# Optimization experiments

Hardware: AMD Instinct MI355X
Metric: run time of the kernel (lower is better)

The kernel has to match this reference:

```python
import jax, jax.numpy as jnp
import numpy as np


def setup_inputs() -> dict:
    key = jax.random.key(0)
    k0, k1, k2, k3 = jax.random.split(key, 4)
    B, N, C, Dout = 4, 8192, 64, 128
    coords = jax.random.normal(k0, (B, N, 3), dtype=jnp.float32)
    features = jax.random.normal(k1, (B, N, C), dtype=jnp.float32)
    W1 = jax.random.normal(k2, (C + 3, Dout), dtype=jnp.float32) / jnp.sqrt(jnp.float32(C + 3))
    b1 = jnp.zeros((Dout,), dtype=jnp.float32)
    W2 = jax.random.normal(k3, (Dout, Dout), dtype=jnp.float32) / jnp.sqrt(jnp.float32(Dout))
    b2 = jnp.zeros((Dout,), dtype=jnp.float32)
    return {"coords": coords, "features": features, "W1": W1, "b1": b1,
            "W2": W2, "b2": b2, "sample_count": 2048, "k": 32}


def reference(coords, features, W1, b1, W2, b2, sample_count, k):
    B, N, _ = coords.shape
    S = min(sample_count, N)
    kk = min(k, N)
    # deterministic linspace centroid sampling (same indices for every batch)
    idx = jnp.round(jnp.linspace(0.0, N - 1, S)).astype(jnp.int32)  # [S]
    sampled = coords[:, idx]  # [B,S,3]
    # squared distances via GEMM (same topk ordering as torch.cdist)
    s2 = jnp.sum(sampled * sampled, axis=-1)          # [B,S]
    c2 = jnp.sum(coords * coords, axis=-1)            # [B,N]
    d2 = s2[:, :, None] + c2[:, None, :] - 2.0 * jnp.einsum('bsd,bnd->bsn', sampled, coords)
    _, knn_idx = jax.lax.top_k(-d2, kk)               # [B,S,kk] smallest distances
    # per-batch irregular gathers
    grouped_c = jax.vmap(lambda c, i: c[i])(coords, knn_idx)      # [B,S,kk,3]
    rel = grouped_c - sampled[:, :, None, :]                      # relative coords
    grouped_f = jax.vmap(lambda f, i: f[i])(features, knn_idx)    # [B,S,kk,C]
    g = jnp.concatenate([rel, grouped_f], axis=-1)                # [B,S,kk,C+3]
    # shared MLP: Linear -> GELU(exact) -> Linear -> GELU(exact)
    h = jax.nn.gelu(g @ W1 + b1, approximate=False)
    h = jax.nn.gelu(h @ W2 + b2, approximate=False)
    pooled = jnp.max(h, axis=2)                                   # [B,S,Dout]
    return sampled, pooled
```

## Files before the change

### kernel.cpp

```cpp
#include <hip/hip_runtime.h>
#include <math.h>

typedef unsigned int u32;
typedef unsigned long long u64;

#define BB 4
#define NN 8192
#define CC 64
#define DOUT 128
#define SS 2048
#define KSEL 32
#define CAPL 2048
#define CAP2 384
#define BREAK_CAP 128

__device__ __forceinline__ int sample_index(int s) {
    if (s == 1706) return 6826;
    const double step = 8191.0 / 2047.0;
    return (int)rint((double)s * step);
}

__device__ __forceinline__ u32 f2s(float f) {
    u32 u = __float_as_uint(f);
    return ((int)u < 0) ? ~u : (u ^ 0x80000000u);
}

__device__ __forceinline__ float gelu(float x) {
    return 0.5f * x * (1.0f + erff(x * 0.70710678118654752f));
}

__global__ __launch_bounds__(256)
__attribute__((amdgpu_waves_per_eu(4, 4)))
void k_select(const float* __restrict__ coords,
              float* __restrict__ out_sampled,
              int* __restrict__ selbuf,
              int selstride) {
    __shared__ __align__(16) u64 cand[CAPL];
    __shared__ __align__(16) u64 cand2[CAP2];
    __shared__ u32 wsum[32];
    __shared__ int sel[KSEL];
    __shared__ int s_nsel, s_ncand, s_n2;

    const int tid = threadIdx.x;
    const int lane = tid & 63;
    const int q = blockIdx.x;
    const int b = q >> 11;
    const int s = q & (SS - 1);
    const int si = sample_index(s);

    const float* cb = coords + (size_t)b * NN * 3;
    const float qx = cb[si * 3 + 0], qy = cb[si * 3 + 1], qz = cb[si * 3 + 2];
    const float q2 = __fadd_rn(__fadd_rn(__fmul_rn(qx, qx), __fmul_rn(qy, qy)), __fmul_rn(qz, qz));

    if (tid == 0) {
        float* dst = out_sampled + (size_t)q * 3;
        dst[0] = qx; dst[1] = qy; dst[2] = qz;
    }

    u32 kr[32];
#pragma unroll
    for (int i = 0; i < 32; i++) {
        int j = tid + (i << 8);
        float x = cb[j * 3 + 0], y = cb[j * 3 + 1], z = cb[j * 3 + 2];
        float n2 = __fadd_rn(__fadd_rn(__fmul_rn(x, x), __fmul_rn(y, y)), __fmul_rn(z, z));
        float dot = __fadd_rn(__fadd_rn(__fmul_rn(qx, x), __fmul_rn(qy, y)), __fmul_rn(qz, z));
        float d2 = __fsub_rn(__fadd_rn(q2, n2), __fmul_rn(2.0f, dot));
        kr[i] = f2s(d2);
    }

#define BFLY_WSUM()                                                          \
    _Pragma("unroll")                                                        \
    for (int w = 0; w < 8; w++) {                                            \
        _Pragma("unroll")                                                    \
        for (int d = 1; d < 64; d <<= 1) cnt[w] += __shfl_xor(cnt[w], d, 64);\
    }                                                                        \
    if ((tid & 63) == 0) {                                                   \
        int wv = tid >> 6;                                                   \
        _Pragma("unroll")                                                    \
        for (int w = 0; w < 8; w++) wsum[wv * 8 + w] = cnt[w];               \
    }                                                                        \
    __syncthreads();

#define SCAN_DIGIT()                                                         \
    u32 tot[8];                                                              \
    _Pragma("unroll")                                                        \
    for (int w = 0; w < 8; w++)                                              \
        tot[w] = wsum[w] + wsum[8 + w] + wsum[16 + w] + wsum[24 + w];        \
    run = 0; D = 15; cc = 0;                                                 \
    _Pragma("unroll")                                                        \
    for (int nib = 0; nib < 16; nib++) {                                     \
        int cv = (nib & 1) ? (int)(tot[nib >> 1] >> 16)                      \
                           : (int)(tot[nib >> 1] & 0xFFFFu);                 \
        if (base + run + cv >= KSEL) { D = nib; cc = cv; break; }            \
        run += cv;                                                           \
    }

    u32 pref = 0;
    int base = 0, shift = 28, c = 0;
    int p = 7;
    {
        u32 cnt[8] = {0, 0, 0, 0, 0, 0, 0, 0};
#pragma unroll
        for (int i = 0; i < 32; i++) {
            u32 nib = kr[i] >> 28;
            cnt[nib >> 1] += 1u << (16 * (nib & 1));
        }
        BFLY_WSUM()
        int run, D, cc;
        SCAN_DIGIT()
        base = run; pref = (u32)D << 28; c = cc;
        __syncthreads();
    }

    while (c > CAPL && p > 0) {
        p--;
        const int sh = 4 * p;
        const u32 hmask = 0xFFFFFFFFu << (sh + 4);
        u32 cnt[8] = {0, 0, 0, 0, 0, 0, 0, 0};
#pragma unroll
        for (int i = 0; i < 32; i++) {
            u32 kv = kr[i];
            if ((kv & hmask) == pref) {
                u32 nib = (kv >> sh) & 15u;
                cnt[nib >> 1] += 1u << (16 * (nib & 1));
            }
        }
        BFLY_WSUM()
        int run, D, cc;
        SCAN_DIGIT()
        base += run; pref |= (u32)D << sh; shift = sh; c = cc;
        __syncthreads();
    }

    if (tid == 0) { s_nsel = 0; s_ncand = 0; }
    __syncthreads();

    const u64 lmlt = (1ull << lane) - 1ull;
    {
        const u32 prefv = pref >> shift;
#pragma unroll
        for (int i = 0; i < 32; i++) {
            int j = tid + (i << 8);
            u32 kv = kr[i];
            u32 kp = kv >> shift;
            bool isS = kp < prefv;
            bool isC = kp == prefv;
            u64 bs = __ballot(isS);
            u64 bc = __ballot(isC);
            int basS = 0, basC = 0;
            if (lane == 0) {
                if (bs) basS = atomicAdd(&s_nsel, (int)__popcll(bs));
                if (bc) basC = atomicAdd(&s_ncand, (int)__popcll(bc));
            }
            basS = __shfl(basS, 0, 64);
            basC = __shfl(basC, 0, 64);
            if (isS) sel[basS + (int)__popcll(bs & lmlt)] = j;
            if (isC) {
                int pos = basC + (int)__popcll(bc & lmlt);
                if (pos < CAPL) cand[pos] = ((u64)kv << 32) | (u32)j;
            }
        }
    }
    __syncthreads();
    int nc = s_ncand; if (nc > CAPL) nc = CAPL;

    int p2 = shift >> 2;
    while (c > BREAK_CAP && p2 > 0) {
        p2--;
        const int sh = 4 * p2;
        const u32 ph = pref >> (sh + 4);
        u32 cnt[8] = {0, 0, 0, 0, 0, 0, 0, 0};
        for (int e = tid; e < nc; e += 256) {
            u32 kv = (u32)(cand[e] >> 32);
            if ((kv >> (sh + 4)) == ph) {
                u32 nib = (kv >> sh) & 15u;
                cnt[nib >> 1] += 1u << (16 * (nib & 1));
            }
        }
        BFLY_WSUM()
        int run, D, cc;
        SCAN_DIGIT()
        base += run; pref |= (u32)D << sh; shift = sh; c = cc;
        __syncthreads();
    }
#undef BFLY_WSUM
#undef SCAN_DIGIT

    if (tid == 0) s_n2 = 0;
    __syncthreads();
    {
        const u32 pv = pref >> shift;
        for (int e = tid; e < nc; e += 256) {
            u64 ent = cand[e];
            u32 kp = (u32)(ent >> 32) >> shift;
            bool isS = kp < pv;
            bool isC = kp == pv;
            u64 bs = __ballot(isS);
            u64 bc = __ballot(isC);
            int basS = 0, basC = 0;
            if (lane == 0) {
                if (bs) basS = atomicAdd(&s_nsel, (int)__popcll(bs));
                if (bc) basC = atomicAdd(&s_n2, (int)__popcll(bc));
            }
            basS = __shfl(basS, 0, 64);
            basC = __shfl(basC, 0, 64);
            if (isS) sel[basS + (int)__popcll(bs & lmlt)] = (int)(ent & 0xFFFFFFFFu);
            if (isC) {
                int pos = basC + (int)__popcll(bc & lmlt);
                if (pos < CAP2) cand2[pos] = ent;
            }
        }
    }
    __syncthreads();

    {
        const int nles = s_nsel;
        const int need = KSEL - nles;
        int n2 = s_n2; if (n2 > CAP2) n2 = CAP2;
        for (int ci = tid; ci < n2; ci += 256) {
            u64 me = cand2[ci];
            int r = 0;
            for (int m = 0; m < n2; m++) r += (cand2[m] < me) ? 1 : 0;
            if (r < need) sel[nles + r] = (int)(me & 0xFFFFFFFFu);
        }
    }
    __syncthreads();

    if (tid < KSEL) selbuf[(size_t)q * selstride + tid] = sel[tid];
}

__global__ __launch_bounds__(512) void k_mlp(const float* __restrict__ coords,
                                             const float* __restrict__ features,
                                             const float* __restrict__ w1,
                                             const float* __restrict__ b1,
                                             const float* __restrict__ w2,
                                             const float* __restrict__ b2,
                                             const int* __restrict__ selbuf,
                                             int selstride,
                                             float* __restrict__ pooled) {
    __shared__ __align__(16) unsigned char smem[32768];
    float* g    = (float*)smem;
    float* h    = (float*)smem;
    float* part = (float*)smem;
    __shared__ int sel2[2][KSEL];

    const int tid = threadIdx.x;
    const int q0 = blockIdx.x << 1;
    const int b = q0 >> 11;
    const float* cb = coords + (size_t)b * NN * 3;

    if (tid < 2 * KSEL) {
        int hq = tid >> 5;
        sel2[hq][tid & 31] = selbuf[(size_t)(q0 + hq) * selstride + (tid & 31)];
    }
    __syncthreads();

    {
        const int hq = tid >> 8;
        const int t = tid & 255;
        const int s = (q0 + hq) & (SS - 1);
        const int si = sample_index(s);
        const float qx = cb[si * 3 + 0], qy = cb[si * 3 + 1], qz = cb[si * 3 + 2];
        const int nbr = (t >> 3) & 31;
        const int cl = t & 7;
        const int n = sel2[hq][nbr];
        const float* fb = features + ((size_t)b * NN + n) * CC;
        float* gq = g + hq * 2144;
#pragma unroll
        for (int m = 0; m < 9; m++) {
            int ch = cl + (m << 3);
            if (ch < 67) {
                float v;
                if (ch < 3) v = cb[n * 3 + ch] - ((ch == 0) ? qx : (ch == 1) ? qy : qz);
                else        v = fb[ch - 3];
                gq[ch * 32 + nbr] = v;
            }
        }
    }
    __syncthreads();

    const int lane = tid & 63;
    const int chb = __builtin_amdgcn_readfirstlane((tid >> 6) << 4);
    const int hq = lane >> 5;
    const int nb = lane & 31;

    float acc[16];

    {
        const float* brow = b1 + chb;
#pragma unroll
        for (int k = 0; k < 16; k++) acc[k] = brow[k];
        const float* aA = g + hq * 2144 + nb;
        const float* w1p = w1 + chb;
        for (int c = 0; c < 67; c++) {
            float a = aA[c * 32];
            const float* wr = w1p + c * DOUT;
#pragma unroll
            for (int k = 0; k < 16; k++) acc[k] = fmaf(a, wr[k], acc[k]);
        }
    }
    __syncthreads();
    {
        float* hp = h + hq * 4096 + nb;
#pragma unroll
        for (int k = 0; k < 16; k++) hp[(chb + k) * 32] = gelu(acc[k]);
    }
    __syncthreads();

    {
        const float* brow = b2 + chb;
#pragma unroll
        for (int k = 0; k < 16; k++) acc[k] = brow[k];
        const float* aA = h + hq * 4096 + nb;
        const float* w2p = w2 + chb;
        for (int c = 0; c < DOUT; c++) {
            float a = aA[c * 32];
            const float* wr = w2p + c * DOUT;
#pragma unroll
            for (int k = 0; k < 16; k++) acc[k] = fmaf(a, wr[k], acc[k]);
        }
    }
#pragma unroll
    for (int k = 0; k < 16; k++) acc[k] = gelu(acc[k]);
    __syncthreads();
    {
        float* pp = part + hq * 4096;
#pragma unroll
        for (int k = 0; k < 16; k++) {
            int j = chb + k;
            pp[j * 32 + (nb ^ (j & 31))] = acc[k];
        }
    }
    __syncthreads();

    if (tid < 256) {
        const int hq2 = tid >> 7;
        const int ch = tid & 127;
        const float* pr = part + hq2 * 4096 + ch * 32;
        const int sw = ch & 31;
        float m = pr[0 ^ sw];
#pragma unroll
        for (int w = 1; w < 32; w++) m = fmaxf(m, pr[w ^ sw]);
        pooled[(size_t)(q0 + hq2) * DOUT + ch] = m;
    }
}

extern "C" void kernel_launch(void* const* d_in, const int* in_sizes, int n_in,
                              void* d_out, int out_size, void* d_ws, size_t ws_size,
                              hipStream_t stream) {
    const float* coords = nullptr;
    const float* features = nullptr;
    const float* W1 = nullptr;
    const float* b1 = nullptr;
    const float* W2 = nullptr;
    const float* b2 = nullptr;
    for (int i = 0; i < n_in; i++) {
        int sz = in_sizes[i];
        const float* p = (const float*)d_in[i];
        if      (sz == BB * NN * 3)     coords = p;
        else if (sz == BB * NN * CC)    features = p;
        else if (sz == (CC + 3) * DOUT) W1 = p;
        else if (sz == DOUT * DOUT)     W2 = p;
        else if (sz == DOUT)            { if (!b1) b1 = p; else b2 = p; }
    }

    float* out_sampled = (float*)d_out;
    float* out_pooled  = (float*)d_out + (size_t)BB * SS * 3;

    const size_t sel_bytes = (size_t)BB * SS * KSEL * sizeof(int);
    int* selbuf;
    int selstride;
    if (ws_size >= sel_bytes && d_ws != nullptr) {
        selbuf = (int*)d_ws;
        selstride = KSEL;
    } else {
        selbuf = (int*)out_pooled;
        selstride = DOUT;
    }

    k_select<<<dim3(BB * SS), dim3(256), 0, stream>>>(coords, out_sampled, selbuf, selstride);
    k_mlp<<<dim3((BB * SS) / 2), dim3(512), 0, stream>>>(coords, features, W1, b1, W2, b2,
                                                         selbuf, selstride, out_pooled);
}
```

Measured before the change: 422.2 us.

## Widen kNN select blocks to 512 threads and use packed FMA in MLP

The top-k selection kernel now runs 512 threads per query instead of 256, so each thread holds 16 distance keys instead of 32, with the per-wave histogram sums widened to 8 waves and the occupancy hints changed. The MLP kernel's accumulators become float2 vectors updated with elementwise FMA, so the compiler can emit packed FP32 FMA instructions. The aim is more parallelism and lower register pressure in selection, and doubled FMA throughput in the MLP. The cost is more barrier and reduction work per block in selection, and a risk that the packed form does not lower to packed instructions.

```diff
diff --git a/kernel.cpp b/kernel.cpp
--- a/kernel.cpp
+++ b/kernel.cpp
@@ -3,6 +3,7 @@
 
 typedef unsigned int u32;
 typedef unsigned long long u64;
+typedef float f32x2 __attribute__((ext_vector_type(2)));
 
 #define BB 4
 #define NN 8192
@@ -29,15 +30,15 @@
     return 0.5f * x * (1.0f + erff(x * 0.70710678118654752f));
 }
 
-__global__ __launch_bounds__(256)
-__attribute__((amdgpu_waves_per_eu(4, 4)))
+__global__ __launch_bounds__(512)
+__attribute__((amdgpu_waves_per_eu(6, 8)))
 void k_select(const float* __restrict__ coords,
               float* __restrict__ out_sampled,
               int* __restrict__ selbuf,
               int selstride) {
     __shared__ __align__(16) u64 cand[CAPL];
     __shared__ __align__(16) u64 cand2[CAP2];
-    __shared__ u32 wsum[32];
+    __shared__ u32 wsum[64];
     __shared__ int sel[KSEL];
     __shared__ int s_nsel, s_ncand, s_n2;
 
@@ -57,10 +58,10 @@
         dst[0] = qx; dst[1] = qy; dst[2] = qz;
     }
 
-    u32 kr[32];
-#pragma unroll
-    for (int i = 0; i < 32; i++) {
-        int j = tid + (i << 8);
+    u32 kr[16];
+#pragma unroll
+    for (int i = 0; i < 16; i++) {
+        int j = tid + (i << 9);
         float x = cb[j * 3 + 0], y = cb[j * 3 + 1], z = cb[j * 3 + 2];
         float n2 = __fadd_rn(__fadd_rn(__fmul_rn(x, x), __fmul_rn(y, y)), __fmul_rn(z, z));
         float dot = __fadd_rn(__fadd_rn(__fmul_rn(qx, x), __fmul_rn(qy, y)), __fmul_rn(qz, z));
@@ -84,8 +85,12 @@
 #define SCAN_DIGIT()                                                         \
     u32 tot[8];                                                              \
     _Pragma("unroll")                                                        \
-    for (int w = 0; w < 8; w++)                                              \
-        tot[w] = wsum[w] + wsum[8 + w] + wsum[16 + w] + wsum[24 + w];        \
+    for (int w = 0; w < 8; w++) {                                            \
+        u32 t = 0;                                                           \
+        _Pragma("unroll")                                                    \
+        for (int v = 0; v < 8; v++) t += wsum[v * 8 + w];                    \
+        tot[w] = t;                                                          \
+    }                                                                        \
     run = 0; D = 15; cc = 0;                                                 \
     _Pragma("unroll")                                                        \
     for (int nib = 0; nib < 16; nib++) {                                     \
@@ -101,7 +106,7 @@
     {
         u32 cnt[8] = {0, 0, 0, 0, 0, 0, 0, 0};
 #pragma unroll
-        for (int i = 0; i < 32; i++) {
+        for (int i = 0; i < 16; i++) {
             u32 nib = kr[i] >> 28;
             cnt[nib >> 1] += 1u << (16 * (nib & 1));
         }
@@ -118,7 +123,7 @@
         const u32 hmask = 0xFFFFFFFFu << (sh + 4);
         u32 cnt[8] = {0, 0, 0, 0, 0, 0, 0, 0};
 #pragma unroll
-        for (int i = 0; i < 32; i++) {
+        for (int i = 0; i < 16; i++) {
             u32 kv = kr[i];
             if ((kv & hmask) == pref) {
                 u32 nib = (kv >> sh) & 15u;
@@ -139,8 +144,8 @@
     {
         const u32 prefv = pref >> shift;
 #pragma unroll
-        for (int i = 0; i < 32; i++) {
-            int j = tid + (i << 8);
+        for (int i = 0; i < 16; i++) {
+            int j = tid + (i << 9);
             u32 kv = kr[i];
             u32 kp = kv >> shift;
             bool isS = kp < prefv;
@@ -170,7 +175,7 @@
         const int sh = 4 * p2;
         const u32 ph = pref >> (sh + 4);
         u32 cnt[8] = {0, 0, 0, 0, 0, 0, 0, 0};
-        for (int e = tid; e < nc; e += 256) {
+        for (int e = tid; e < nc; e += 512) {
             u32 kv = (u32)(cand[e] >> 32);
             if ((kv >> (sh + 4)) == ph) {
                 u32 nib = (kv >> sh) & 15u;
@@ -190,7 +195,7 @@
     __syncthreads();
     {
         const u32 pv = pref >> shift;
-        for (int e = tid; e < nc; e += 256) {
+        for (int e = tid; e < nc; e += 512) {
             u64 ent = cand[e];
             u32 kp = (u32)(ent >> 32) >> shift;
             bool isS = kp < pv;
@@ -217,7 +222,7 @@
         const int nles = s_nsel;
         const int need = KSEL - nles;
         int n2 = s_n2; if (n2 > CAP2) n2 = CAP2;
-        for (int ci = tid; ci < n2; ci += 256) {
+        for (int ci = tid; ci < n2; ci += 512) {
             u64 me = cand2[ci];
             int r = 0;
             for (int m = 0; m < n2; m++) r += (cand2[m] < me) ? 1 : 0;
@@ -284,51 +289,58 @@
     const int hq = lane >> 5;
     const int nb = lane & 31;
 
-    float acc[16];
-
-    {
-        const float* brow = b1 + chb;
-#pragma unroll
-        for (int k = 0; k < 16; k++) acc[k] = brow[k];
+    f32x2 acc2[8];
+
+    {
+        const f32x2* br2 = (const f32x2*)(b1 + chb);
+#pragma unroll
+        for (int k = 0; k < 8; k++) acc2[k] = br2[k];
         const float* aA = g + hq * 2144 + nb;
         const float* w1p = w1 + chb;
         for (int c = 0; c < 67; c++) {
             float a = aA[c * 32];
-            const float* wr = w1p + c * DOUT;
-#pragma unroll
-            for (int k = 0; k < 16; k++) acc[k] = fmaf(a, wr[k], acc[k]);
+            f32x2 av = {a, a};
+            const f32x2* wr2 = (const f32x2*)(w1p + c * DOUT);
+#pragma unroll
+            for (int k = 0; k < 8; k++)
+                acc2[k] = __builtin_elementwise_fma(av, wr2[k], acc2[k]);
         }
     }
     __syncthreads();
     {
         float* hp = h + hq * 4096 + nb;
 #pragma unroll
-        for (int k = 0; k < 16; k++) hp[(chb + k) * 32] = gelu(acc[k]);
-    }
-    __syncthreads();
-
-    {
-        const float* brow = b2 + chb;
-#pragma unroll
-        for (int k = 0; k < 16; k++) acc[k] = brow[k];
+        for (int k = 0; k < 8; k++) {
+            hp[(chb + 2 * k) * 32]     = gelu(acc2[k].x);
+            hp[(chb + 2 * k + 1) * 32] = gelu(acc2[k].y);
+        }
+    }
+    __syncthreads();
+
+    {
+        const f32x2* br2 = (const f32x2*)(b2 + chb);
+#pragma unroll
+        for (int k = 0; k < 8; k++) acc2[k] = br2[k];
         const float* aA = h + hq * 4096 + nb;
         const float* w2p = w2 + chb;
         for (int c = 0; c < DOUT; c++) {
             float a = aA[c * 32];
-            const float* wr = w2p + c * DOUT;
-#pragma unroll
-            for (int k = 0; k < 16; k++) acc[k] = fmaf(a, wr[k], acc[k]);
-        }
-    }
-#pragma unroll
-    for (int k = 0; k < 16; k++) acc[k] = gelu(acc[k]);
+            f32x2 av = {a, a};
+            const f32x2* wr2 = (const f32x2*)(w2p + c * DOUT);
+#pragma unroll
+            for (int k = 0; k < 8; k++)
+                acc2[k] = __builtin_elementwise_fma(av, wr2[k], acc2[k]);
+        }
+    }
     __syncthreads();
     {
         float* pp = part + hq * 4096;
 #pragma unroll
-        for (int k = 0; k < 16; k++) {
-            int j = chb + k;
-            pp[j * 32 + (nb ^ (j & 31))] = acc[k];
+        for (int k = 0; k < 8; k++) {
+            int j0 = chb + 2 * k;
+            int j1 = j0 + 1;
+            pp[j0 * 32 + (nb ^ (j0 & 31))] = gelu(acc2[k].x);
+            pp[j1 * 32 + (nb ^ (j1 & 31))] = gelu(acc2[k].y);
         }
     }
     __syncthreads();
@@ -378,7 +390,7 @@
         selstride = DOUT;
     }
 
-    k_select<<<dim3(BB * SS), dim3(256), 0, stream>>>(coords, out_sampled, selbuf, selstride);
+    k_select<<<dim3(BB * SS), dim3(512), 0, stream>>>(coords, out_sampled, selbuf, selstride);
     k_mlp<<<dim3((BB * SS) / 2), dim3(512), 0, stream>>>(coords, features, W1, b1, W2, b2,
                                                          selbuf, selstride, out_pooled);
 }
```

Result: slower. 445.4 us (+5.5%).
